# Performance work log

Hardware: AMD Instinct MI355X
Metric: run time of the kernel (lower is better)

Reference implementation:

```python
import jax, jax.numpy as jnp
import numpy as np

B, IN_DIM, HID, N_WIRES = 8192, 2048, 2048, 8


def setup_inputs() -> dict:
    key = jax.random.key(0)
    ks = jax.random.split(key, 12)
    fan_in = IN_DIM + HID
    w_scale = 1.0 / np.sqrt(fan_in)  # ~ nn.Linear default init scale
    mk_w = lambda k: jax.random.normal(k, (N_WIRES, fan_in), jnp.float32) * w_scale
    mk_b = lambda k: jax.random.normal(k, (N_WIRES,), jnp.float32) * w_scale
    return {
        "x": jax.random.normal(ks[0], (B, IN_DIM), jnp.float32),
        "hx": jax.random.normal(ks[1], (B, HID), jnp.float32),
        "cx": jax.random.normal(ks[2], (B, HID), jnp.float32),
        "Wf": mk_w(ks[3]), "bf": mk_b(ks[4]),
        "Wi": mk_w(ks[5]), "bi": mk_b(ks[6]),
        "Wg": mk_w(ks[7]), "bg": mk_b(ks[8]),
        "Wo": mk_w(ks[9]), "bo": mk_b(ks[10]),
    }


def reference(x, hx, cx, Wf, bf, Wi, bi, Wg, bg, Wo, bo):
    combined = jnp.concatenate([x, hx], axis=1)  # [B, IN+HID]
    # Exact expectation of the RX-only circuit: E[#zeros - #ones] = sum_i cos(angle_i)
    q_exp = lambda W, b: jnp.sum(jnp.cos(combined @ W.T + b))
    f = jax.nn.sigmoid(q_exp(Wf, bf))
    i = jax.nn.sigmoid(q_exp(Wi, bi))
    g = jnp.tanh(q_exp(Wg, bg))
    o = jax.nn.sigmoid(q_exp(Wo, bo))
    cx_new = f * cx + i * g
    hx_new = o * jnp.tanh(cx_new)
    return hx_new, cx_new
```

## Files before the change

### kernel.cpp

```cpp
#include <hip/hip_runtime.h>
#include <hip/hip_bf16.h>
#include <cstdint>
#include <cstddef>

#define B_ROWS 8192
#define KDIM   4096
#define IN_DIM 2048
#define HIDDEN 2048
#define NJ     32
#define KC     8
#define CHUNK  (KDIM / KC)
#define BK     64
#define SUBT   (CHUNK / BK)
#define MROWS  32
#define TPB1   128
#define NBUF   4

typedef __bf16 bf16x8 __attribute__((ext_vector_type(8)));
typedef __bf16 bf16x4 __attribute__((ext_vector_type(4)));
typedef float  f32x4  __attribute__((ext_vector_type(4)));

__device__ __forceinline__ bf16x8 cvt8(f32x4 a, f32x4 b) {
    bf16x8 r;
    r[0] = (__bf16)a.x; r[1] = (__bf16)a.y; r[2] = (__bf16)a.z; r[3] = (__bf16)a.w;
    r[4] = (__bf16)b.x; r[5] = (__bf16)b.y; r[6] = (__bf16)b.z; r[7] = (__bf16)b.w;
    return r;
}

__device__ __forceinline__ void gload_lds16(const void* g, void* lds) {
    __builtin_amdgcn_global_load_lds(
        (const __attribute__((address_space(1))) void*)g,
        (__attribute__((address_space(3))) void*)lds, 16, 0, 0);
}

extern "C" __global__ __launch_bounds__(256)
void w_pack(const float* __restrict__ Wf, const float* __restrict__ Wi,
            const float* __restrict__ Wg, const float* __restrict__ Wo,
            __bf16* __restrict__ Wb, float* __restrict__ q)
{
    if (blockIdx.x == 0 && threadIdx.x < 4) q[threadIdx.x] = 0.f;

    const int t    = blockIdx.x * 256 + threadIdx.x;
    const int idx4 = t << 2;
    const int j    = idx4 >> 12;
    const int k    = idx4 & (KDIM - 1);
    const float* W = (j < 8) ? Wf : (j < 16) ? Wi : (j < 24) ? Wg : Wo;
    f32x4 v = *reinterpret_cast<const f32x4*>(W + (size_t)(j & 7) * KDIM + k);
    bf16x4 b;
    b[0] = (__bf16)v.x; b[1] = (__bf16)v.y; b[2] = (__bf16)v.z; b[3] = (__bf16)v.w;
    *reinterpret_cast<bf16x4*>(Wb + idx4) = b;
}

extern "C" __global__ __launch_bounds__(TPB1)
void p1_mfma(const float* __restrict__ x, const float* __restrict__ hx,
             const __bf16* __restrict__ Wb, float* __restrict__ Spart)
{
    __shared__ float  Abuf[NBUF][MROWS * BK];
    __shared__ __bf16 Bbuf[NBUF][NJ * BK];

    const int bid  = blockIdx.x;
    const int kc   = bid & (KC - 1);
    const int mb   = bid >> 3;
    const int tid  = threadIdx.x;
    const int wave = tid >> 6;
    const int lane = tid & 63;
    const int lrow = lane & 15;
    const int rowblk = mb * MROWS;
    const int k0   = kc * CHUNK;

    const float* Aglob = (kc < 4)
        ? (x  + (size_t)rowblk * IN_DIM + k0)
        : (hx + (size_t)rowblk * HIDDEN + (k0 - IN_DIM));
    const __bf16* Bglob = Wb + k0;

    int aOff[4];
#pragma unroll
    for (int p = 0; p < 4; ++p) {
        const int r  = (wave * 4 + p) * 4 + (lane >> 4);
        const int cs = (lane & 15) ^ (r & 7);
        aOff[p] = r * 2048 + cs * 4;
    }
    int bOff[2];
#pragma unroll
    for (int i = 0; i < 2; ++i) {
        const int j = (wave * 2 + i) * 8 + (lane >> 3);
        bOff[i] = j * KDIM + (((lane & 7) ^ (j & 7)) * 8);
    }

    const int row_r = wave * 16 + lrow;
    int offA0[2], offA1[2], offB0[2], offB1[2];
#pragma unroll
    for (int st = 0; st < 2; ++st) {
        const int cu = st * 8 + (lane >> 4) * 2;
        offA0[st] = row_r * 256 + ((cu + 0) ^ (lane & 7)) * 16;
        offA1[st] = row_r * 256 + ((cu + 1) ^ (lane & 7)) * 16;
        const int cb = st * 4 + (lane >> 4);
        offB0[st] = lrow * 128        + (cb ^ (lrow & 7)) * 16;
        offB1[st] = (lrow + 16) * 128 + (cb ^ (lrow & 7)) * 16;
    }

    f32x4 acc0 = {0.f, 0.f, 0.f, 0.f};
    f32x4 acc1 = {0.f, 0.f, 0.f, 0.f};

    auto issue = [&](int s) {
        const int b = s & (NBUF - 1);
#pragma unroll
        for (int p = 0; p < 4; ++p)
            gload_lds16(Aglob + aOff[p] + s * BK, &Abuf[b][(wave * 4 + p) * 256]);
#pragma unroll
        for (int i = 0; i < 2; ++i)
            gload_lds16(Bglob + bOff[i] + s * BK, &Bbuf[b][(wave * 2 + i) * 512]);
    };
    auto compute = [&](int s) {
        const int b = s & (NBUF - 1);
        const char* Ab = (const char*)&Abuf[b][0];
        const char* Bb = (const char*)&Bbuf[b][0];
#pragma unroll
        for (int st = 0; st < 2; ++st) {
            f32x4 a0 = *reinterpret_cast<const f32x4*>(Ab + offA0[st]);
            f32x4 a1 = *reinterpret_cast<const f32x4*>(Ab + offA1[st]);
            bf16x8 af = cvt8(a0, a1);
            bf16x8 b0 = *reinterpret_cast<const bf16x8*>(Bb + offB0[st]);
            bf16x8 b1 = *reinterpret_cast<const bf16x8*>(Bb + offB1[st]);
            acc0 = __builtin_amdgcn_mfma_f32_16x16x32_bf16(af, b0, acc0, 0, 0, 0);
            acc1 = __builtin_amdgcn_mfma_f32_16x16x32_bf16(af, b1, acc1, 0, 0, 0);
        }
    };

    issue(0);
    issue(1);
#pragma unroll
    for (int s = 0; s < SUBT; ++s) {
        if (s + 2 < SUBT) issue(s + 2);
        if (s < SUBT - 2)
            asm volatile("s_waitcnt vmcnt(12)" ::: "memory");
        else if (s == SUBT - 2)
            asm volatile("s_waitcnt vmcnt(6)" ::: "memory");
        else
            asm volatile("s_waitcnt vmcnt(0)" ::: "memory");
        __builtin_amdgcn_s_barrier();
        __builtin_amdgcn_sched_barrier(0);
        compute(s);
    }

    const int row0 = rowblk + wave * 16;
    float* sp = Spart + ((size_t)kc * B_ROWS + row0) * NJ;
    const int m0 = (lane >> 4) * 4;
#pragma unroll
    for (int r = 0; r < 4; ++r) {
        sp[(size_t)(m0 + r) * NJ + lrow]      = acc0[r];
        sp[(size_t)(m0 + r) * NJ + 16 + lrow] = acc1[r];
    }
}

extern "C" __global__ __launch_bounds__(256)
void p2_cos_reduce(const float* __restrict__ Spart,
                   const float* __restrict__ bf, const float* __restrict__ bi,
                   const float* __restrict__ bg, const float* __restrict__ bo,
                   float* __restrict__ q)
{
    __shared__ float ql[4];
    if (threadIdx.x < 4) ql[threadIdx.x] = 0.f;
    __syncthreads();

    const int t    = blockIdx.x * 256 + threadIdx.x;
    const int j    = t & 31;
    const int gate = j >> 3;
    const float* Bp = (gate == 0) ? bf : (gate == 1) ? bi : (gate == 2) ? bg : bo;
    const float bj = Bp[j & 7];

    float accg = 0.f;
#pragma unroll
    for (int i = 0; i < 4; ++i) {
        const int row = (t >> 5) + i * 2048;
        float s = 0.f;
#pragma unroll
        for (int kc = 0; kc < KC; ++kc)
            s += Spart[((size_t)kc * B_ROWS + row) * NJ + j];
        accg += cosf(s + bj);
    }

    accg += __shfl_xor(accg, 1, 64);
    accg += __shfl_xor(accg, 2, 64);
    accg += __shfl_xor(accg, 4, 64);
    if ((threadIdx.x & 7) == 0) atomicAdd(&ql[gate], accg);
    __syncthreads();
    if (threadIdx.x < 4) atomicAdd(&q[threadIdx.x], ql[threadIdx.x]);
}

extern "C" __global__ __launch_bounds__(256)
void p3_elementwise(const float* __restrict__ cx, const float* __restrict__ q,
                    float* __restrict__ out)
{
    const float qf = q[0], qi = q[1], qg = q[2], qo = q[3];
    const float f  = 1.f / (1.f + expf(-qf));
    const float ii = 1.f / (1.f + expf(-qi));
    const float g  = tanhf(qg);
    const float o  = 1.f / (1.f + expf(-qo));
    const float ig = ii * g;

    const size_t N  = (size_t)B_ROWS * HIDDEN;
    const size_t N4 = N >> 2;
    const f32x4* cx4 = (const f32x4*)cx;
    f32x4* outh = (f32x4*)out;
    f32x4* outc = (f32x4*)(out + N);

    for (size_t idx = (size_t)blockIdx.x * blockDim.x + threadIdx.x; idx < N4;
         idx += (size_t)gridDim.x * blockDim.x) {
        f32x4 c = __builtin_nontemporal_load(cx4 + idx);
        f32x4 cn, hn;
        cn.x = fmaf(f, c.x, ig);
        cn.y = fmaf(f, c.y, ig);
        cn.z = fmaf(f, c.z, ig);
        cn.w = fmaf(f, c.w, ig);
        hn.x = o * tanhf(cn.x);
        hn.y = o * tanhf(cn.y);
        hn.z = o * tanhf(cn.z);
        hn.w = o * tanhf(cn.w);
        outc[idx] = cn;
        outh[idx] = hn;
    }
}

extern "C" void kernel_launch(void* const* d_in, const int* in_sizes, int n_in,
                              void* d_out, int out_size, void* d_ws, size_t ws_size,
                              hipStream_t stream)
{
    const float* x  = (const float*)d_in[0];
    const float* hx = (const float*)d_in[1];
    const float* cx = (const float*)d_in[2];
    const float* Wf = (const float*)d_in[3];
    const float* bf = (const float*)d_in[4];
    const float* Wi = (const float*)d_in[5];
    const float* bi = (const float*)d_in[6];
    const float* Wg = (const float*)d_in[7];
    const float* bg = (const float*)d_in[8];
    const float* Wo = (const float*)d_in[9];
    const float* bo = (const float*)d_in[10];
    float* out = (float*)d_out;

    float*   Spart = (float*)d_ws;
    __bf16*  Wb    = (__bf16*)(Spart + (size_t)KC * B_ROWS * NJ);
    float*   q     = (float*)(Wb + (size_t)NJ * KDIM);

    w_pack<<<dim3(128), dim3(256), 0, stream>>>(Wf, Wi, Wg, Wo, Wb, q);
    p1_mfma<<<dim3(256 * KC), dim3(TPB1), 0, stream>>>(x, hx, Wb, Spart);
    p2_cos_reduce<<<dim3(256), dim3(256), 0, stream>>>(Spart, bf, bi, bg, bo, q);
    p3_elementwise<<<dim3(2048), dim3(256), 0, stream>>>(cx, q, out);
}
```

Before: 78.10 us.

## Retile MFMA pass to single-wave blocks with deeper prefetch and nontemporal stores

The GEMM pass now uses one 64-thread wave per block covering 16 rows. It splits K into 4 chunks instead of 8, which halves the partial sums the reduction has to read. Each block prefetches three stages ahead and drops the block barrier, since only one wave touches the LDS buffers. The elementwise pass moves its nontemporal hint from the cx load to the two output stores. The trade-offs are fewer waves per block to hide latency, more sequential K work per block, and weight tiles being reloaded by twice as many blocks.

After: 69.82 us. 1.12x faster.

```diff
diff --git a/kernel.cpp b/kernel.cpp
--- a/kernel.cpp
+++ b/kernel.cpp
@@ -8,12 +8,12 @@
 #define IN_DIM 2048
 #define HIDDEN 2048
 #define NJ     32
-#define KC     8
+#define KC     4
 #define CHUNK  (KDIM / KC)
 #define BK     64
 #define SUBT   (CHUNK / BK)
-#define MROWS  32
-#define TPB1   128
+#define MROWS  16
+#define TPB1   64
 #define NBUF   4
 
 typedef __bf16 bf16x8 __attribute__((ext_vector_type(8)));
@@ -60,15 +60,13 @@
 
     const int bid  = blockIdx.x;
     const int kc   = bid & (KC - 1);
-    const int mb   = bid >> 3;
-    const int tid  = threadIdx.x;
-    const int wave = tid >> 6;
-    const int lane = tid & 63;
+    const int mb   = bid >> 2;
+    const int lane = threadIdx.x & 63;
     const int lrow = lane & 15;
     const int rowblk = mb * MROWS;
     const int k0   = kc * CHUNK;
 
-    const float* Aglob = (kc < 4)
+    const float* Aglob = (kc < 2)
         ? (x  + (size_t)rowblk * IN_DIM + k0)
         : (hx + (size_t)rowblk * HIDDEN + (k0 - IN_DIM));
     const __bf16* Bglob = Wb + k0;
@@ -76,27 +74,26 @@
     int aOff[4];
 #pragma unroll
     for (int p = 0; p < 4; ++p) {
-        const int r  = (wave * 4 + p) * 4 + (lane >> 4);
+        const int r  = p * 4 + (lane >> 4);
         const int cs = (lane & 15) ^ (r & 7);
         aOff[p] = r * 2048 + cs * 4;
     }
-    int bOff[2];
-#pragma unroll
-    for (int i = 0; i < 2; ++i) {
-        const int j = (wave * 2 + i) * 8 + (lane >> 3);
+    int bOff[4];
+#pragma unroll
+    for (int i = 0; i < 4; ++i) {
+        const int j = i * 8 + (lane >> 3);
         bOff[i] = j * KDIM + (((lane & 7) ^ (j & 7)) * 8);
     }
 
-    const int row_r = wave * 16 + lrow;
     int offA0[2], offA1[2], offB0[2], offB1[2];
 #pragma unroll
     for (int st = 0; st < 2; ++st) {
         const int cu = st * 8 + (lane >> 4) * 2;
-        offA0[st] = row_r * 256 + ((cu + 0) ^ (lane & 7)) * 16;
-        offA1[st] = row_r * 256 + ((cu + 1) ^ (lane & 7)) * 16;
+        offA0[st] = lrow * 256 + (((cu + 0) ^ (lane & 7)) * 16);
+        offA1[st] = lrow * 256 + (((cu + 1) ^ (lane & 7)) * 16);
         const int cb = st * 4 + (lane >> 4);
-        offB0[st] = lrow * 128        + (cb ^ (lrow & 7)) * 16;
-        offB1[st] = (lrow + 16) * 128 + (cb ^ (lrow & 7)) * 16;
+        offB0[st] = lrow * 128        + ((cb ^ (lrow & 7)) * 16);
+        offB1[st] = (lrow + 16) * 128 + ((cb ^ (lrow & 7)) * 16);
     }
 
     f32x4 acc0 = {0.f, 0.f, 0.f, 0.f};
@@ -106,10 +103,10 @@
         const int b = s & (NBUF - 1);
 #pragma unroll
         for (int p = 0; p < 4; ++p)
-            gload_lds16(Aglob + aOff[p] + s * BK, &Abuf[b][(wave * 4 + p) * 256]);
-#pragma unroll
-        for (int i = 0; i < 2; ++i)
-            gload_lds16(Bglob + bOff[i] + s * BK, &Bbuf[b][(wave * 2 + i) * 512]);
+            gload_lds16(Aglob + aOff[p] + s * BK, &Abuf[b][p * 256]);
+#pragma unroll
+        for (int i = 0; i < 4; ++i)
+            gload_lds16(Bglob + bOff[i] + s * BK, &Bbuf[b][i * 512]);
     };
     auto compute = [&](int s) {
         const int b = s & (NBUF - 1);
@@ -129,22 +126,23 @@
 
     issue(0);
     issue(1);
+    issue(2);
 #pragma unroll
     for (int s = 0; s < SUBT; ++s) {
-        if (s + 2 < SUBT) issue(s + 2);
-        if (s < SUBT - 2)
-            asm volatile("s_waitcnt vmcnt(12)" ::: "memory");
+        if (s + 3 < SUBT) issue(s + 3);
+        if (s < SUBT - 3)
+            asm volatile("s_waitcnt vmcnt(24)" ::: "memory");
+        else if (s == SUBT - 3)
+            asm volatile("s_waitcnt vmcnt(16)" ::: "memory");
         else if (s == SUBT - 2)
-            asm volatile("s_waitcnt vmcnt(6)" ::: "memory");
+            asm volatile("s_waitcnt vmcnt(8)" ::: "memory");
         else
             asm volatile("s_waitcnt vmcnt(0)" ::: "memory");
-        __builtin_amdgcn_s_barrier();
         __builtin_amdgcn_sched_barrier(0);
         compute(s);
     }
 
-    const int row0 = rowblk + wave * 16;
-    float* sp = Spart + ((size_t)kc * B_ROWS + row0) * NJ;
+    float* sp = Spart + ((size_t)kc * B_ROWS + rowblk) * NJ;
     const int m0 = (lane >> 4) * 4;
 #pragma unroll
     for (int r = 0; r < 4; ++r) {
@@ -207,7 +205,7 @@
 
     for (size_t idx = (size_t)blockIdx.x * blockDim.x + threadIdx.x; idx < N4;
          idx += (size_t)gridDim.x * blockDim.x) {
-        f32x4 c = __builtin_nontemporal_load(cx4 + idx);
+        f32x4 c = cx4[idx];
         f32x4 cn, hn;
         cn.x = fmaf(f, c.x, ig);
         cn.y = fmaf(f, c.y, ig);
@@ -217,8 +215,8 @@
         hn.y = o * tanhf(cn.y);
         hn.z = o * tanhf(cn.z);
         hn.w = o * tanhf(cn.w);
-        outc[idx] = cn;
-        outh[idx] = hn;
+        __builtin_nontemporal_store(cn, outc + idx);
+        __builtin_nontemporal_store(hn, outh + idx);
     }
 }
 
@@ -244,7 +242,7 @@
     float*   q     = (float*)(Wb + (size_t)NJ * KDIM);
 
     w_pack<<<dim3(128), dim3(256), 0, stream>>>(Wf, Wi, Wg, Wo, Wb, q);
-    p1_mfma<<<dim3(256 * KC), dim3(TPB1), 0, stream>>>(x, hx, Wb, Spart);
+    p1_mfma<<<dim3(512 * KC), dim3(TPB1), 0, stream>>>(x, hx, Wb, Spart);
     p2_cos_reduce<<<dim3(256), dim3(256), 0, stream>>>(Spart, bf, bi, bg, bo, q);
     p3_elementwise<<<dim3(2048), dim3(256), 0, stream>>>(cx, q, out);
 }
```
